# Kernel tuning notes

Hardware: AMD Instinct MI355X
Metric: run time of the kernel (lower is better)

Reference implementation:

```python
import jax, jax.numpy as jnp
import numpy as np

S = 8192  # sequence length
D = 256   # feature dim


def setup_inputs() -> dict:
    key = jax.random.key(0)
    kq, kk, kv = jax.random.split(key, 3)
    Q = jax.random.normal(kq, (S, D), dtype=jnp.float32)
    K = jax.random.normal(kk, (S, D), dtype=jnp.float32)
    V = jax.random.normal(kv, (S, D), dtype=jnp.float32)
    return {"Q": Q, "K": K, "V": V}


def reference(Q, K, V):
    # Faithful to the torch module: dk = K.size(-2) (the SEQUENCE length, not head dim)
    dk = K.shape[-2]
    scores = (Q @ K.T) / jnp.sqrt(jnp.float32(dk))  # [S, S]
    # F.softmax with implicit dim on a 2D tensor -> softmax over last dim (keys)
    attn = jax.nn.softmax(scores, axis=-1)
    return attn @ V  # [S, D]
```

## Files before the change

kernel.cpp:

```cpp
#include <hip/hip_runtime.h>


typedef __attribute__((ext_vector_type(4))) float    f32x4;
typedef __attribute__((ext_vector_type(4))) int      i32x4;
typedef __attribute__((ext_vector_type(4))) _Float16 h4;
typedef __attribute__((ext_vector_type(8))) _Float16 h8;
typedef long __attribute__((may_alias)) long_a;
typedef i32x4 __attribute__((may_alias)) i32x4_a;
typedef h8    __attribute__((may_alias)) h8_a;

#define SEQ 8192
#define DIM 256
#define NSPLIT 8
#define KPS (SEQ / NSPLIT)
#define BN 32
#define ITERS (KPS / BN)
#define BM 128

#define KSC (1.4426950408889634f / 90.50966799187808f)

__global__ void __launch_bounds__(256)
prep(const float* __restrict__ Q, const float* __restrict__ K,
     const float* __restrict__ V, unsigned char* __restrict__ Q8,
     unsigned char* __restrict__ K8, _Float16* __restrict__ Vt) {
    __shared__ _Float16 tile[32][264];
    int b = blockIdx.x, t = threadIdx.x;

    {
        int row = b * 32 + (t >> 3);
        int c0 = (t & 7) * 8;
        const f32x4* q4 = (const f32x4*)Q + (size_t)row * 64 + c0;
        const f32x4* k4 = (const f32x4*)K + (size_t)row * 64 + c0;
        int qo[8], ko[8];
        #pragma unroll
        for (int i = 0; i < 8; ++i) {
            f32x4 q = q4[i], k = k4[i];
            int dq = 0, dk = 0;
            dq = __builtin_amdgcn_cvt_pk_fp8_f32(q.x, q.y, dq, false);
            dq = __builtin_amdgcn_cvt_pk_fp8_f32(q.z, q.w, dq, true);
            dk = __builtin_amdgcn_cvt_pk_fp8_f32(k.x, k.y, dk, false);
            dk = __builtin_amdgcn_cvt_pk_fp8_f32(k.z, k.w, dk, true);
            qo[i] = dq; ko[i] = dk;
        }
        i32x4* qd = (i32x4*)(Q8 + (size_t)row * 256 + (t & 7) * 32);
        i32x4* kd = (i32x4*)(K8 + (size_t)row * 256 + (t & 7) * 32);
        qd[0] = *(i32x4*)&qo[0]; qd[1] = *(i32x4*)&qo[4];
        kd[0] = *(i32x4*)&ko[0]; kd[1] = *(i32x4*)&ko[4];
    }

    #pragma unroll
    for (int i = 0; i < 8; ++i) {
        int c = t + i * 256;
        int row = c >> 6, col = c & 63;
        f32x4 v = ((const f32x4*)V)[(size_t)(b * 32 + row) * 64 + col];
        tile[row][col * 4 + 0] = (_Float16)v.x;
        tile[row][col * 4 + 1] = (_Float16)v.y;
        tile[row][col * 4 + 2] = (_Float16)v.z;
        tile[row][col * 4 + 3] = (_Float16)v.w;
    }
    __syncthreads();
    _Float16* dst = Vt + (size_t)b * 8192 + t * 32;
    #pragma unroll
    for (int a = 0; a < 4; ++a) {
        h8 w;
        #pragma unroll
        for (int j = 0; j < 4; ++j) {
            w[j]     = tile[4 * a + j][t];
            w[4 + j] = tile[16 + 4 * a + j][t];
        }
        *(h8*)(dst + a * 8) = w;
    }
}

__global__ void __launch_bounds__(256, 2)
attn(const unsigned char* __restrict__ Q8, const unsigned char* __restrict__ K8,
     const _Float16* __restrict__ Vt, _Float16* __restrict__ Op,
     float* __restrict__ lp) {
    __shared__ unsigned char K_lds[2][32][272];
    __shared__ _Float16 V_lds[2][256][40];

    int tid = threadIdx.x;
    int wid = tid >> 6, lane = tid & 63;
    int l15 = lane & 15, qq = lane >> 4;
    int qt_blk = blockIdx.x >> 3, sp = blockIdx.x & 7;
    int qrow0 = qt_blk * BM + wid * 32;

    long qf[2][8];
    #pragma unroll
    for (int t = 0; t < 2; ++t) {
        const unsigned char* p = Q8 + (size_t)(qrow0 + t * 16 + l15) * DIM + qq * 8;
        #pragma unroll
        for (int s = 0; s < 8; ++s) qf[t][s] = *(const long_a*)(p + s * 32);
    }

    _Float16 one = (l15 == 0) ? (_Float16)1.0f : (_Float16)0.0f;
    h8 of = {one, one, one, one, one, one, one, one};

    const unsigned char* ksrc = K8 + (size_t)(sp * KPS + (tid >> 4)) * DIM + (tid & 15) * 16;
    const _Float16* vsrc = Vt + (size_t)sp * (KPS / BN) * 8192 + (tid >> 2) * 32 + (tid & 3) * 8;
    int kr = tid >> 4, kc = (tid & 15) * 16;
    int vr = tid >> 2, vc = (tid & 3) * 8;

    f32x4 acc[2][16] = {};
    f32x4 accl[2] = {};
    i32x4 kreg[2];
    h8 vreg[4];

    kreg[0] = *(const i32x4_a*)ksrc;
    kreg[1] = *(const i32x4_a*)(ksrc + 16 * DIM);
    #pragma unroll
    for (int p = 0; p < 4; ++p) vreg[p] = *(const h8_a*)(vsrc + p * 64 * 32);
    ksrc += BN * DIM; vsrc += 8192;
    *(i32x4_a*)&K_lds[0][kr][kc]      = kreg[0];
    *(i32x4_a*)&K_lds[0][kr + 16][kc] = kreg[1];
    #pragma unroll
    for (int p = 0; p < 4; ++p) *(h8_a*)&V_lds[0][vr + p * 64][vc] = vreg[p];
    __syncthreads();

    for (int it = 0; it < ITERS; ++it) {
        int b = it & 1;
        if (it + 1 < ITERS) {
            kreg[0] = *(const i32x4_a*)ksrc;
            kreg[1] = *(const i32x4_a*)(ksrc + 16 * DIM);
            #pragma unroll
            for (int p = 0; p < 4; ++p) vreg[p] = *(const h8_a*)(vsrc + p * 64 * 32);
            ksrc += BN * DIM; vsrc += 8192;
        }

        f32x4 sc[2][2] = {};
        #pragma unroll
        for (int s = 0; s < 8; ++s) {
            long kf0 = *(const long_a*)&K_lds[b][l15][s * 32 + qq * 8];
            long kf1 = *(const long_a*)&K_lds[b][16 + l15][s * 32 + qq * 8];
            #pragma unroll
            for (int t = 0; t < 2; ++t) {
                sc[0][t] = __builtin_amdgcn_mfma_f32_16x16x32_fp8_fp8(kf0, qf[t][s], sc[0][t], 0, 0, 0);
                sc[1][t] = __builtin_amdgcn_mfma_f32_16x16x32_fp8_fp8(kf1, qf[t][s], sc[1][t], 0, 0, 0);
            }
        }

        h8 pfrag[2];
        #pragma unroll
        for (int t = 0; t < 2; ++t)
            #pragma unroll
            for (int r = 0; r < 4; ++r) {
                pfrag[t][r]     = (_Float16)__builtin_amdgcn_exp2f(fminf(sc[0][t][r] * KSC, 16.0f));
                pfrag[t][4 + r] = (_Float16)__builtin_amdgcn_exp2f(fminf(sc[1][t][r] * KSC, 16.0f));
            }

        #pragma unroll
        for (int n = 0; n < 16; ++n) {
            h8 vf = *(const h8_a*)&V_lds[b][n * 16 + l15][qq * 8];
            acc[0][n] = __builtin_amdgcn_mfma_f32_16x16x32_f16(pfrag[0], vf, acc[0][n], 0, 0, 0);
            acc[1][n] = __builtin_amdgcn_mfma_f32_16x16x32_f16(pfrag[1], vf, acc[1][n], 0, 0, 0);
        }
        accl[0] = __builtin_amdgcn_mfma_f32_16x16x32_f16(pfrag[0], of, accl[0], 0, 0, 0);
        accl[1] = __builtin_amdgcn_mfma_f32_16x16x32_f16(pfrag[1], of, accl[1], 0, 0, 0);

        if (it + 1 < ITERS) {
            int nb = b ^ 1;
            *(i32x4_a*)&K_lds[nb][kr][kc]      = kreg[0];
            *(i32x4_a*)&K_lds[nb][kr + 16][kc] = kreg[1];
            #pragma unroll
            for (int p = 0; p < 4; ++p) *(h8_a*)&V_lds[nb][vr + p * 64][vc] = vreg[p];
            __syncthreads();
        }
    }

    #pragma unroll
    for (int t = 0; t < 2; ++t) {
        #pragma unroll
        for (int n = 0; n < 16; ++n)
            #pragma unroll
            for (int r = 0; r < 4; ++r) {
                int row = qrow0 + t * 16 + qq * 4 + r;
                Op[((size_t)sp * SEQ + row) * DIM + n * 16 + l15] = (_Float16)acc[t][n][r];
            }
        if (l15 == 0) {
            #pragma unroll
            for (int r = 0; r < 4; ++r)
                lp[(size_t)sp * SEQ + qrow0 + t * 16 + qq * 4 + r] = accl[t][r];
        }
    }
}

__global__ void combine(const _Float16* __restrict__ Op, const float* __restrict__ lp,
                        float* __restrict__ out) {
    int idx = blockIdx.x * 256 + threadIdx.x;
    int row = idx >> 6;
    f32x4 a = {};
    float l = 0.0f;
    #pragma unroll
    for (int s = 0; s < NSPLIT; ++s) {
        h4 h = *(const h4*)(Op + (size_t)s * SEQ * DIM + (size_t)idx * 4);
        a.x += (float)h.x; a.y += (float)h.y; a.z += (float)h.z; a.w += (float)h.w;
        l += lp[s * SEQ + row];
    }
    float linv = 1.0f / (l + 1e-20f);
    ((f32x4*)out)[idx] = a * linv;
}

extern "C" void kernel_launch(void* const* d_in, const int* in_sizes, int n_in,
                              void* d_out, int out_size, void* d_ws, size_t ws_size,
                              hipStream_t stream) {
    const float* Q = (const float*)d_in[0];
    const float* K = (const float*)d_in[1];
    const float* V = (const float*)d_in[2];
    float* out = (float*)d_out;

    char* ws = (char*)d_ws;
    unsigned char* Q8 = (unsigned char*)ws;
    unsigned char* K8 = (unsigned char*)(ws + (2u << 20));
    _Float16* Vt = (_Float16*)(ws + (4u << 20));
    _Float16* Op = (_Float16*)(ws + (8u << 20));
    float*    lp = (float*)(ws + (40u << 20));

    prep   <<<256, 256, 0, stream>>>(Q, K, V, Q8, K8, Vt);
    attn   <<<NSPLIT * (SEQ / BM), 256, 0, stream>>>(Q8, K8, Vt, Op, lp);
    combine<<<2048, 256, 0, stream>>>(Op, lp, out);
}
```

Measured before the change: 142.3 us.

## Triple-buffer K/V via direct global-to-LDS loads and software-pipeline QK ahead of PV

Re-lays out K8 and Vt in prep into MFMA-fragment-ordered tiles, so the attention kernel can stream them straight into LDS with global_load_lds instead of staging through registers. It uses a three-buffer ring and computes the next tile's QK scores while the current tile's softmax-PV runs, raising wave priority around the MFMA section. P is packed with cvt_pkrtz, and combine now handles 8 halves per thread. The aim is to hide load latency and cut register and VGPR pressure from staged loads, at the cost of more LDS use (72KB), which may limit occupancy, and a more fragile layout contract between the prep and attention kernels.

After: 140.0 us. No clear change (-1.6%).

```diff
diff --git a/kernel.cpp b/kernel.cpp
--- a/kernel.cpp
+++ b/kernel.cpp
@@ -3,10 +3,12 @@
 
 typedef __attribute__((ext_vector_type(4))) float    f32x4;
 typedef __attribute__((ext_vector_type(4))) int      i32x4;
-typedef __attribute__((ext_vector_type(4))) _Float16 h4;
+typedef __attribute__((ext_vector_type(2))) long     lx2;
+typedef __attribute__((ext_vector_type(2))) _Float16 h2;
+typedef __attribute__((ext_vector_type(2))) __fp16   h2raw;
 typedef __attribute__((ext_vector_type(8))) _Float16 h8;
-typedef long __attribute__((may_alias)) long_a;
-typedef i32x4 __attribute__((may_alias)) i32x4_a;
+typedef long  __attribute__((may_alias)) long_a;
+typedef lx2   __attribute__((may_alias)) lx2_a;
 typedef h8    __attribute__((may_alias)) h8_a;
 
 #define SEQ 8192
@@ -18,6 +20,10 @@
 #define BM 128
 
 #define KSC (1.4426950408889634f / 90.50966799187808f)
+
+#define KTILE 8192
+#define VTILE 16384
+#define BUFSZ (KTILE + VTILE)
 
 __global__ void __launch_bounds__(256)
 prep(const float* __restrict__ Q, const float* __restrict__ K,
@@ -43,9 +49,13 @@
             qo[i] = dq; ko[i] = dk;
         }
         i32x4* qd = (i32x4*)(Q8 + (size_t)row * 256 + (t & 7) * 32);
-        i32x4* kd = (i32x4*)(K8 + (size_t)row * 256 + (t & 7) * 32);
         qd[0] = *(i32x4*)&qo[0]; qd[1] = *(i32x4*)&qo[4];
-        kd[0] = *(i32x4*)&ko[0]; kd[1] = *(i32x4*)&ko[4];
+
+        int s16h = (((t & 7) >> 1) << 1) + (t >> 7);
+        long* kdst = (long*)(K8 + (size_t)b * KTILE + (size_t)s16h * 1024
+                             + (size_t)((t >> 3) & 15) * 16 + (size_t)(t & 1) * 8);
+        #pragma unroll
+        for (int q = 0; q < 4; ++q) kdst[q * 32] = *(const long*)&ko[2 * q];
     }
 
     #pragma unroll
@@ -59,7 +69,7 @@
         tile[row][col * 4 + 3] = (_Float16)v.w;
     }
     __syncthreads();
-    _Float16* dst = Vt + (size_t)b * 8192 + t * 32;
+    _Float16* dst = Vt + (size_t)b * 8192 + (size_t)t * 8;
     #pragma unroll
     for (int a = 0; a < 4; ++a) {
         h8 w;
@@ -68,20 +78,61 @@
             w[j]     = tile[4 * a + j][t];
             w[4 + j] = tile[16 + 4 * a + j][t];
         }
-        *(h8*)(dst + a * 8) = w;
-    }
-}
+        *(h8_a*)(dst + (size_t)a * 2048) = w;
+    }
+}
+
+__device__ __forceinline__ void gl16(const void* g, void* l) {
+    __builtin_amdgcn_global_load_lds(
+        (const __attribute__((address_space(1))) void*)g,
+        (__attribute__((address_space(3))) void*)l, 16, 0, 0);
+}
+
+__device__ __forceinline__ h2 pkrtz(float a, float b) {
+    h2raw r = __builtin_amdgcn_cvt_pkrtz(a, b);
+    return __builtin_bit_cast(h2, r);
+}
+
+__device__ __forceinline__ void qk32(const unsigned char* kb, int koff,
+                                     const long (&qf)[2][8], f32x4 (&sc)[2][2]) {
+    #pragma unroll
+    for (int h = 0; h < 2; ++h)
+        #pragma unroll
+        for (int t = 0; t < 2; ++t) sc[h][t] = (f32x4){0.f, 0.f, 0.f, 0.f};
+    #pragma unroll
+    for (int s16 = 0; s16 < 4; ++s16) {
+        #pragma unroll
+        for (int h = 0; h < 2; ++h) {
+            lx2 kp = *(const lx2_a*)(kb + (s16 * 2 + h) * 1024 + koff);
+            #pragma unroll
+            for (int t = 0; t < 2; ++t) {
+                sc[h][t] = __builtin_amdgcn_mfma_f32_16x16x32_fp8_fp8(kp[0], qf[t][2 * s16],     sc[h][t], 0, 0, 0);
+                sc[h][t] = __builtin_amdgcn_mfma_f32_16x16x32_fp8_fp8(kp[1], qf[t][2 * s16 + 1], sc[h][t], 0, 0, 0);
+            }
+        }
+    }
+}
+
+#define STAGE(KG, VG, BUF)                                                   \
+    do {                                                                     \
+        gl16((KG) + tid * 16,           (BUF) + wb);                         \
+        gl16((KG) + 4096 + tid * 16,    (BUF) + 4096 + wb);                  \
+        gl16((VG) + tid * 16,           (BUF) + KTILE + wb);                 \
+        gl16((VG) + 4096 + tid * 16,    (BUF) + KTILE + 4096 + wb);         \
+        gl16((VG) + 8192 + tid * 16,    (BUF) + KTILE + 8192 + wb);         \
+        gl16((VG) + 12288 + tid * 16,   (BUF) + KTILE + 12288 + wb);        \
+    } while (0)
 
 __global__ void __launch_bounds__(256, 2)
 attn(const unsigned char* __restrict__ Q8, const unsigned char* __restrict__ K8,
      const _Float16* __restrict__ Vt, _Float16* __restrict__ Op,
      float* __restrict__ lp) {
-    __shared__ unsigned char K_lds[2][32][272];
-    __shared__ _Float16 V_lds[2][256][40];
+    __shared__ __align__(16) unsigned char lds[3 * BUFSZ];
 
     int tid = threadIdx.x;
     int wid = tid >> 6, lane = tid & 63;
     int l15 = lane & 15, qq = lane >> 4;
+    int wb = wid << 10;
     int qt_blk = blockIdx.x >> 3, sp = blockIdx.x & 7;
     int qrow0 = qt_blk * BM + wid * 32;
 
@@ -96,75 +147,72 @@
     _Float16 one = (l15 == 0) ? (_Float16)1.0f : (_Float16)0.0f;
     h8 of = {one, one, one, one, one, one, one, one};
 
-    const unsigned char* ksrc = K8 + (size_t)(sp * KPS + (tid >> 4)) * DIM + (tid & 15) * 16;
-    const _Float16* vsrc = Vt + (size_t)sp * (KPS / BN) * 8192 + (tid >> 2) * 32 + (tid & 3) * 8;
-    int kr = tid >> 4, kc = (tid & 15) * 16;
-    int vr = tid >> 2, vc = (tid & 3) * 8;
+    unsigned char* bufA = lds;
+    unsigned char* bufB = lds + BUFSZ;
+    unsigned char* bufC = lds + 2 * BUFSZ;
+
+    const unsigned char* kg = K8 + (size_t)sp * ITERS * KTILE;
+    const unsigned char* vg = (const unsigned char*)Vt + (size_t)sp * ITERS * VTILE;
 
     f32x4 acc[2][16] = {};
     f32x4 accl[2] = {};
-    i32x4 kreg[2];
-    h8 vreg[4];
-
-    kreg[0] = *(const i32x4_a*)ksrc;
-    kreg[1] = *(const i32x4_a*)(ksrc + 16 * DIM);
-    #pragma unroll
-    for (int p = 0; p < 4; ++p) vreg[p] = *(const h8_a*)(vsrc + p * 64 * 32);
-    ksrc += BN * DIM; vsrc += 8192;
-    *(i32x4_a*)&K_lds[0][kr][kc]      = kreg[0];
-    *(i32x4_a*)&K_lds[0][kr + 16][kc] = kreg[1];
-    #pragma unroll
-    for (int p = 0; p < 4; ++p) *(h8_a*)&V_lds[0][vr + p * 64][vc] = vreg[p];
+
+    int koff = qq * 256 + l15 * 16;
+    int voff = qq * 4096 + l15 * 16;
+
+    STAGE(kg, vg, bufA); kg += KTILE; vg += VTILE;
+    STAGE(kg, vg, bufB); kg += KTILE; vg += VTILE;
     __syncthreads();
+    f32x4 sc_p[2][2];
+    qk32(bufA, koff, qf, sc_p);
 
     for (int it = 0; it < ITERS; ++it) {
-        int b = it & 1;
-        if (it + 1 < ITERS) {
-            kreg[0] = *(const i32x4_a*)ksrc;
-            kreg[1] = *(const i32x4_a*)(ksrc + 16 * DIM);
-            #pragma unroll
-            for (int p = 0; p < 4; ++p) vreg[p] = *(const h8_a*)(vsrc + p * 64 * 32);
-            ksrc += BN * DIM; vsrc += 8192;
-        }
-
-        f32x4 sc[2][2] = {};
-        #pragma unroll
-        for (int s = 0; s < 8; ++s) {
-            long kf0 = *(const long_a*)&K_lds[b][l15][s * 32 + qq * 8];
-            long kf1 = *(const long_a*)&K_lds[b][16 + l15][s * 32 + qq * 8];
-            #pragma unroll
-            for (int t = 0; t < 2; ++t) {
-                sc[0][t] = __builtin_amdgcn_mfma_f32_16x16x32_fp8_fp8(kf0, qf[t][s], sc[0][t], 0, 0, 0);
-                sc[1][t] = __builtin_amdgcn_mfma_f32_16x16x32_fp8_fp8(kf1, qf[t][s], sc[1][t], 0, 0, 0);
-            }
-        }
+        if (it + 2 < ITERS) { STAGE(kg, vg, bufC); kg += KTILE; vg += VTILE; }
+
+        __builtin_amdgcn_s_setprio(1);
+
+        f32x4 sc_n[2][2] = {};
+        if (it + 1 < ITERS) qk32(bufB, koff, qf, sc_n);
 
         h8 pfrag[2];
         #pragma unroll
-        for (int t = 0; t < 2; ++t)
-            #pragma unroll
-            for (int r = 0; r < 4; ++r) {
-                pfrag[t][r]     = (_Float16)__builtin_amdgcn_exp2f(fminf(sc[0][t][r] * KSC, 16.0f));
-                pfrag[t][4 + r] = (_Float16)__builtin_amdgcn_exp2f(fminf(sc[1][t][r] * KSC, 16.0f));
-            }
-
+        for (int t = 0; t < 2; ++t) {
+            float e0 = __builtin_amdgcn_exp2f(fminf(sc_p[0][t][0] * KSC, 16.0f));
+            float e1 = __builtin_amdgcn_exp2f(fminf(sc_p[0][t][1] * KSC, 16.0f));
+            float e2 = __builtin_amdgcn_exp2f(fminf(sc_p[0][t][2] * KSC, 16.0f));
+            float e3 = __builtin_amdgcn_exp2f(fminf(sc_p[0][t][3] * KSC, 16.0f));
+            float e4 = __builtin_amdgcn_exp2f(fminf(sc_p[1][t][0] * KSC, 16.0f));
+            float e5 = __builtin_amdgcn_exp2f(fminf(sc_p[1][t][1] * KSC, 16.0f));
+            float e6 = __builtin_amdgcn_exp2f(fminf(sc_p[1][t][2] * KSC, 16.0f));
+            float e7 = __builtin_amdgcn_exp2f(fminf(sc_p[1][t][3] * KSC, 16.0f));
+            h2 p01 = pkrtz(e0, e1);
+            h2 p23 = pkrtz(e2, e3);
+            h2 p45 = pkrtz(e4, e5);
+            h2 p67 = pkrtz(e6, e7);
+            h8 pf;
+            pf[0] = p01[0]; pf[1] = p01[1]; pf[2] = p23[0]; pf[3] = p23[1];
+            pf[4] = p45[0]; pf[5] = p45[1]; pf[6] = p67[0]; pf[7] = p67[1];
+            pfrag[t] = pf;
+        }
+
+        const unsigned char* vb = bufA + KTILE + voff;
         #pragma unroll
         for (int n = 0; n < 16; ++n) {
-            h8 vf = *(const h8_a*)&V_lds[b][n * 16 + l15][qq * 8];
+            h8 vf = *(const h8_a*)(vb + n * 256);
             acc[0][n] = __builtin_amdgcn_mfma_f32_16x16x32_f16(pfrag[0], vf, acc[0][n], 0, 0, 0);
             acc[1][n] = __builtin_amdgcn_mfma_f32_16x16x32_f16(pfrag[1], vf, acc[1][n], 0, 0, 0);
         }
         accl[0] = __builtin_amdgcn_mfma_f32_16x16x32_f16(pfrag[0], of, accl[0], 0, 0, 0);
         accl[1] = __builtin_amdgcn_mfma_f32_16x16x32_f16(pfrag[1], of, accl[1], 0, 0, 0);
 
-        if (it + 1 < ITERS) {
-            int nb = b ^ 1;
-            *(i32x4_a*)&K_lds[nb][kr][kc]      = kreg[0];
-            *(i32x4_a*)&K_lds[nb][kr + 16][kc] = kreg[1];
-            #pragma unroll
-            for (int p = 0; p < 4; ++p) *(h8_a*)&V_lds[nb][vr + p * 64][vc] = vreg[p];
-            __syncthreads();
-        }
+        __builtin_amdgcn_s_setprio(0);
+        __syncthreads();
+
+        unsigned char* tb = bufA; bufA = bufB; bufB = bufC; bufC = tb;
+        #pragma unroll
+        for (int h = 0; h < 2; ++h)
+            #pragma unroll
+            for (int t = 0; t < 2; ++t) sc_p[h][t] = sc_n[h][t];
     }
 
     #pragma unroll
@@ -184,20 +232,25 @@
     }
 }
 
-__global__ void combine(const _Float16* __restrict__ Op, const float* __restrict__ lp,
-                        float* __restrict__ out) {
+__global__ void __launch_bounds__(256)
+combine(const _Float16* __restrict__ Op, const float* __restrict__ lp,
+        float* __restrict__ out) {
     int idx = blockIdx.x * 256 + threadIdx.x;
-    int row = idx >> 6;
-    f32x4 a = {};
+    int row = idx >> 5;
+    f32x4 a0 = {}, a1 = {};
     float l = 0.0f;
     #pragma unroll
     for (int s = 0; s < NSPLIT; ++s) {
-        h4 h = *(const h4*)(Op + (size_t)s * SEQ * DIM + (size_t)idx * 4);
-        a.x += (float)h.x; a.y += (float)h.y; a.z += (float)h.z; a.w += (float)h.w;
+        h8 h = *(const h8_a*)(Op + (size_t)s * SEQ * DIM + (size_t)idx * 8);
+        a0.x += (float)h[0]; a0.y += (float)h[1];
+        a0.z += (float)h[2]; a0.w += (float)h[3];
+        a1.x += (float)h[4]; a1.y += (float)h[5];
+        a1.z += (float)h[6]; a1.w += (float)h[7];
         l += lp[s * SEQ + row];
     }
     float linv = 1.0f / (l + 1e-20f);
-    ((f32x4*)out)[idx] = a * linv;
+    ((f32x4*)out)[idx * 2]     = a0 * linv;
+    ((f32x4*)out)[idx * 2 + 1] = a1 * linv;
 }
 
 extern "C" void kernel_launch(void* const* d_in, const int* in_sizes, int n_in,
@@ -217,5 +270,5 @@
 
     prep   <<<256, 256, 0, stream>>>(Q, K, V, Q8, K8, Vt);
     attn   <<<NSPLIT * (SEQ / BM), 256, 0, stream>>>(Q8, K8, Vt, Op, lp);
-    combine<<<2048, 256, 0, stream>>>(Op, lp, out);
-}
+    combine<<<1024, 256, 0, stream>>>(Op, lp, out);
+}
```
